# Optimization experiments

Hardware: AMD Instinct MI355X
Metric: run time of the kernel (lower is better)

## Reference

```python
import jax, jax.numpy as jnp
import numpy as np

D_MODEL, N_HEAD, D_FFN = 1024, 16, 4096
MAX_REL = 128
NUM_BUCKETS = 2 * MAX_REL - 1  # 255
B, T = 2, 2048


def algebraic_ln(x, gamma, beta, a, b_raw, eps=1e-5):
    mean = jnp.mean(x, axis=-1, keepdims=True)
    var = jnp.var(x, axis=-1, keepdims=True)  # unbiased=False
    z = var + eps
    b = jax.nn.softplus(10.0 * b_raw) / 10.0  # softplus with beta=10
    p = a[0] + a[1] * z + a[2] * z ** 2
    q = b[0] + b[1] * z + b[2] * z ** 2
    return (x - mean) * (p / q) * gamma + beta


def setup_inputs() -> dict:
    key = jax.random.key(0)
    ks = jax.random.split(key, 16)
    s = (1.0 / np.sqrt(D_MODEL)).astype(np.float32)
    inp = {
        'x': jax.random.normal(ks[0], (B, T, D_MODEL), jnp.float32),
        'casual_mask': jnp.tril(jnp.ones((T, T), dtype=bool)),
        'Wq': jax.random.normal(ks[1], (D_MODEL, D_MODEL), jnp.float32) * s,
        'bq': jnp.zeros((D_MODEL,), jnp.float32),
        'Wk': jax.random.normal(ks[2], (D_MODEL, D_MODEL), jnp.float32) * s,
        'bk': jnp.zeros((D_MODEL,), jnp.float32),
        'Wv': jax.random.normal(ks[3], (D_MODEL, D_MODEL), jnp.float32) * s,
        'bv': jnp.zeros((D_MODEL,), jnp.float32),
        'Wo': jax.random.normal(ks[4], (D_MODEL, D_MODEL), jnp.float32) * s,
        'bo': jnp.zeros((D_MODEL,), jnp.float32),
        'rel_emb': jax.random.normal(ks[5], (NUM_BUCKETS, N_HEAD), jnp.float32) * 0.02,
        'g1': jnp.ones((D_MODEL,), jnp.float32),
        'be1': jnp.zeros((D_MODEL,), jnp.float32),
        'a1': jnp.array([1.0, 0.5, 0.1], jnp.float32),
        'br1': jnp.array([1.0, 0.3, 0.05], jnp.float32),
        'g2': jnp.ones((D_MODEL,), jnp.float32),
        'be2': jnp.zeros((D_MODEL,), jnp.float32),
        'a2': jnp.array([1.0, 0.5, 0.1], jnp.float32),
        'br2': jnp.array([1.0, 0.3, 0.05], jnp.float32),
        'W1': jax.random.normal(ks[6], (D_FFN, D_MODEL), jnp.float32) * s,
        'b1': jnp.zeros((D_FFN,), jnp.float32),
        'W2': jax.random.normal(ks[7], (D_MODEL, D_FFN), jnp.float32) * (1.0 / np.sqrt(D_FFN)),
        'b2': jnp.zeros((D_MODEL,), jnp.float32),
        'res_scale': jnp.array(0.5, jnp.float32),
    }
    return inp


def attention(x, mask, Wq, bq, Wk, bk, Wv, bv, Wo, bo, rel_emb):
    Bx, Tx, C = x.shape
    H, Dh = N_HEAD, C // N_HEAD
    scale = Dh ** -0.5
    Q = (x @ Wq.T + bq).reshape(Bx, Tx, H, Dh)
    K = (x @ Wk.T + bk).reshape(Bx, Tx, H, Dh)
    V = (x @ Wv.T + bv).reshape(Bx, Tx, H, Dh)
    scores = jnp.einsum('bqhd,bkhd->bhqk', Q, K) * scale
    rel = jnp.arange(Tx)[None, :] - jnp.arange(Tx)[:, None]  # k_pos - q_pos
    buckets = jnp.clip(rel, -MAX_REL + 1, MAX_REL - 1) + (MAX_REL - 1)
    bias = rel_emb[buckets]  # [T,T,H]
    scores = scores + jnp.transpose(bias, (2, 0, 1))[None]
    m = mask[None, None]  # [1,1,T,T]
    # torch: masked_fill(-inf) then masked_fill(0) -> masked entries become 0
    scores = jnp.where(m, scores, 0.0)
    w = jax.nn.relu(scores) + 1e-6
    w = jnp.where(m, w, 0.0)
    w = w / (jnp.sum(w, axis=-1, keepdims=True) + 1e-6)
    out = jnp.einsum('bhqk,bkhd->bqhd', w, V).reshape(Bx, Tx, C)
    return out @ Wo.T + bo


def reference(x, casual_mask, Wq, bq, Wk, bk, Wv, bv, Wo, bo, rel_emb,
              g1, be1, a1, br1, g2, be2, a2, br2, W1, b1, W2, b2, res_scale):
    scale = jnp.clip(res_scale, 0.2, 1.0)
    x = x + scale * attention(algebraic_ln(x, g1, be1, a1, br1), casual_mask,
                              Wq, bq, Wk, bk, Wv, bv, Wo, bo, rel_emb)
    h = algebraic_ln(x, g2, be2, a2, br2)
    ffn = jax.nn.relu(h @ W1.T + b1) @ W2.T + b2  # dropout is identity at eval
    return x + scale * ffn
```

## Files before the change

kernel.cpp:

```cpp
#include <hip/hip_runtime.h>
#include <stdint.h>


#define D_MODEL 1024
#define T_SEQ   2048
#define NHEAD   16
#define DH      64
#define DFFN    4096
#define MROWS   4096

using short8  = __attribute__((ext_vector_type(8))) short;
using floatx4 = __attribute__((ext_vector_type(4))) float;

__device__ __forceinline__ float bf2f(ushort u) {
    union { uint32_t i; float f; } x; x.i = ((uint32_t)u) << 16; return x.f;
}
__device__ __forceinline__ ushort f2bf(float f) {
    union { float f; uint32_t i; } x; x.f = f;
    uint32_t i = x.i;
    return (ushort)((i + 0x7fffu + ((i >> 16) & 1u)) >> 16);
}
__device__ __forceinline__ float ldf(const void* p, size_t i, int dt) {
    return dt ? bf2f(((const ushort*)p)[i]) : ((const float*)p)[i];
}
__device__ __forceinline__ int detect_bf16(const void* g1) {
    return *(const uint32_t*)g1 == 0x3F803F80u;
}
__device__ __forceinline__ void gld_lds16(const void* g, void* l) {
    __builtin_amdgcn_global_load_lds(
        (__attribute__((address_space(1))) uint32_t*)(g),
        (__attribute__((address_space(3))) uint32_t*)(l), 16, 0, 0);
}
__device__ __forceinline__ float softplus10(float t) {
    float u = 10.f * t;
    return (u > 20.f ? u : log1pf(expf(u))) * 0.1f;
}

template <int INMODE>
__global__ __launch_bounds__(256)
void ln_kernel(const void* __restrict__ xin,
               const void* __restrict__ gamma, const void* __restrict__ beta,
               const void* __restrict__ a3, const void* __restrict__ br3,
               ushort* __restrict__ out, const void* __restrict__ dtprobe,
               const void* __restrict__ b2fold, const void* __restrict__ scale_p)
{
    const int dt = detect_bf16(dtprobe);
    const int row = blockIdx.x;
    const int tid = threadIdx.x;
    const int col = tid * 4;
    float v[4];
    if (INMODE >= 1) {
        const float* x = (const float*)xin + (size_t)row * D_MODEL;
        float4 t = *(const float4*)(x + col);
        v[0] = t.x; v[1] = t.y; v[2] = t.z; v[3] = t.w;
    } else if (dt) {
        const ushort* x = (const ushort*)xin + (size_t)row * D_MODEL;
        ushort4 t = *(const ushort4*)(x + col);
        v[0] = bf2f(t.x); v[1] = bf2f(t.y); v[2] = bf2f(t.z); v[3] = bf2f(t.w);
    } else {
        const float* x = (const float*)xin + (size_t)row * D_MODEL;
        float4 t = *(const float4*)(x + col);
        v[0] = t.x; v[1] = t.y; v[2] = t.z; v[3] = t.w;
    }
    float s  = v[0] + v[1] + v[2] + v[3];
    float s2 = v[0]*v[0] + v[1]*v[1] + v[2]*v[2] + v[3]*v[3];
#pragma unroll
    for (int m = 32; m > 0; m >>= 1) {
        s  += __shfl_down(s,  m, 64);
        s2 += __shfl_down(s2, m, 64);
    }
    __shared__ float wsum[4], wsum2[4];
    const int wave = tid >> 6, lane = tid & 63;
    if (lane == 0) { wsum[wave] = s; wsum2[wave] = s2; }
    __syncthreads();
    s  = wsum[0] + wsum[1] + wsum[2] + wsum[3];
    s2 = wsum2[0] + wsum2[1] + wsum2[2] + wsum2[3];
    const float mean = s * (1.f / D_MODEL);
    const float var  = s2 * (1.f / D_MODEL) - mean * mean;
    const float z = var + 1e-5f;
    const float a0 = ldf(a3, 0, dt), a1 = ldf(a3, 1, dt), a2 = ldf(a3, 2, dt);
    const float b0 = softplus10(ldf(br3, 0, dt));
    const float b1 = softplus10(ldf(br3, 1, dt));
    const float b2 = softplus10(ldf(br3, 2, dt));
    const float p = a0 + a1 * z + a2 * z * z;
    const float q = b0 + b1 * z + b2 * z * z;
    const float f = p / q;
    ushort4 o; ushort* op = (ushort*)&o;
#pragma unroll
    for (int e = 0; e < 4; e++) {
        op[e] = f2bf((v[e] - mean) * f * ldf(gamma, col + e, dt) + ldf(beta, col + e, dt));
    }
    *(ushort4*)(out + (size_t)row * D_MODEL + col) = o;
    if (INMODE == 2) {
        const float scl = fminf(fmaxf(ldf(scale_p, 0, dt), 0.2f), 1.0f);
        float* xw = (float*)xin + (size_t)row * D_MODEL;
        float4 t;
        t.x = v[0] + scl * ldf(b2fold, col + 0, dt);
        t.y = v[1] + scl * ldf(b2fold, col + 1, dt);
        t.z = v[2] + scl * ldf(b2fold, col + 2, dt);
        t.w = v[3] + scl * ldf(b2fold, col + 3, dt);
        *(float4*)(xw + col) = t;
    }
}

__global__ __launch_bounds__(256)
void cast_out(const float* __restrict__ x1, void* __restrict__ out,
              const void* __restrict__ dtprobe)
{
    const int dt = detect_bf16(dtprobe);
    const int row = blockIdx.x;
    const int col = threadIdx.x * 4;
    float4 t = *(const float4*)(x1 + (size_t)row * D_MODEL + col);
    if (dt) {
        ushort4 o;
        o.x = f2bf(t.x); o.y = f2bf(t.y); o.z = f2bf(t.z); o.w = f2bf(t.w);
        *(ushort4*)((ushort*)out + (size_t)row * D_MODEL + col) = o;
    } else {
        *(float4*)((float*)out + (size_t)row * D_MODEL + col) = t;
    }
}

template <int MODE, int BM, int BN>
__global__ __launch_bounds__(256)
void gemm_bt(const ushort* __restrict__ A,
             const void* __restrict__ Bw0, const void* __restrict__ Bw1,
             const void* __restrict__ Bw2,
             const void* __restrict__ bias0, const void* __restrict__ bias1,
             const void* __restrict__ bias2,
             void* __restrict__ C0, void* __restrict__ C1, void* __restrict__ C2v,
             int Nst, int K, const void* __restrict__ dtprobe)
{
    constexpr int NI = BM / 32;
    constexpr int NJ = BN / 32;
    constexpr int AC = BM / 64;
    constexpr int BC = BN / 64;
    __shared__ __align__(16) ushort As[BM * 32];
    __shared__ __align__(16) ushort Bs[BN * 32];
    const int dt = detect_bf16(dtprobe);
    const int tid  = threadIdx.x;
    const int wave = tid >> 6, lane = tid & 63;
    const int wr = wave >> 1, wc = wave & 1;
    const int g = lane >> 4, l15 = lane & 15;

    const void* Bw = Bw0; const void* bias = bias0; void* Cout = C0;
    if (MODE == 4) {
        const int mat = blockIdx.x >> 3;
        if (mat == 1)      { Bw = Bw1; bias = bias1; Cout = C1; }
        else if (mat == 2) { Bw = Bw2; bias = bias2; Cout = C2v; }
    }
    const int m0 = blockIdx.y * BM;
    const int n0 = (MODE == 4) ? ((blockIdx.x & 7) * 128) : (blockIdx.x * BN);

    floatx4 acc[NI][NJ];
#pragma unroll
    for (int i = 0; i < NI; i++)
#pragma unroll
        for (int j = 0; j < NJ; j++) acc[i][j] = {0.f, 0.f, 0.f, 0.f};

    const int srow = lane >> 2;
    const int ssw  = (srow >> 1) & 3;
    const int scol = (((lane & 3) ^ ssw) * 8);
    const int fsw  = (l15 >> 1) & 3;
    for (int k0 = 0; k0 < K; k0 += 32) {
        __syncthreads();
        if (dt) {
            const ushort* Bb = (const ushort*)Bw;
#pragma unroll
            for (int c = 0; c < AC; c++) {
                const int r0 = (wave * AC + c) * 16;
                gld_lds16(A + (size_t)(m0 + r0 + srow) * K + k0 + scol, &As[r0 * 32]);
            }
#pragma unroll
            for (int c = 0; c < BC; c++) {
                const int r0 = (wave * BC + c) * 16;
                gld_lds16(Bb + (size_t)(n0 + r0 + srow) * K + k0 + scol, &Bs[r0 * 32]);
            }
        } else {
            const float* Bf = (const float*)Bw;
#pragma unroll
            for (int c = 0; c < AC; c++) {
                const int r0 = (wave * AC + c) * 16;
                gld_lds16(A + (size_t)(m0 + r0 + srow) * K + k0 + scol, &As[r0 * 32]);
            }
#pragma unroll
            for (int c = 0; c < BC; c++) {
                const int r0 = (wave * BC + c) * 16;
                const float* src = Bf + (size_t)(n0 + r0 + srow) * K + k0 + scol;
                float4 t0 = *(const float4*)(src);
                float4 t1 = *(const float4*)(src + 4);
                ushort tmp[8] = { f2bf(t0.x), f2bf(t0.y), f2bf(t0.z), f2bf(t0.w),
                                  f2bf(t1.x), f2bf(t1.y), f2bf(t1.z), f2bf(t1.w) };
                *(short8*)&Bs[(r0 + srow) * 32 + (lane & 3) * 8] = *(short8*)tmp;
            }
        }
        __syncthreads();
        short8 af[NI], bfr[NJ];
#pragma unroll
        for (int i = 0; i < NI; i++)
            af[i]  = *(const short8*)&As[(wr * (BM / 2) + i * 16 + l15) * 32 + ((g ^ fsw) * 8)];
#pragma unroll
        for (int j = 0; j < NJ; j++)
            bfr[j] = *(const short8*)&Bs[(wc * (BN / 2) + j * 16 + l15) * 32 + ((g ^ fsw) * 8)];
#pragma unroll
        for (int i = 0; i < NI; i++)
#pragma unroll
            for (int j = 0; j < NJ; j++)
                acc[i][j] = __builtin_amdgcn_mfma_f32_16x16x32_bf16(af[i], bfr[j], acc[i][j], 0, 0, 0);
    }

#pragma unroll
    for (int i = 0; i < NI; i++) {
        const int rowb = m0 + wr * (BM / 2) + i * 16 + g * 4;
#pragma unroll
        for (int j = 0; j < NJ; j++) {
            const int col = n0 + wc * (BN / 2) + j * 16 + l15;
            const float bi = ldf(bias, col, dt);
#pragma unroll
            for (int r = 0; r < 4; r++) {
                const size_t idx = (size_t)(rowb + r) * Nst + col;
                const float v = acc[i][j][r] + bi;
                if (MODE == 1) ((ushort*)Cout)[idx] = f2bf(fmaxf(v, 0.f));
                else           ((ushort*)Cout)[idx] = f2bf(v);
            }
        }
    }
}

template <int MODE>
__global__ __launch_bounds__(256)
void gemm_k64p(const ushort* __restrict__ A, const void* __restrict__ Bw,
               const void* __restrict__ bias, void* __restrict__ Cout,
               const void* __restrict__ resid, const void* __restrict__ scale_p,
               int Nst, int K, const void* __restrict__ dtprobe)
{
    __shared__ __align__(16) ushort As[2][2][64 * 32];
    __shared__ __align__(16) ushort Bs[2][2][64 * 32];
    const int dt = detect_bf16(dtprobe);
    const int tid  = threadIdx.x;
    const int wave = tid >> 6, lane = tid & 63;
    const int wr = wave >> 1, wc = wave & 1;
    const int g = lane >> 4, l15 = lane & 15;
    const int m0 = blockIdx.y * 64, n0 = blockIdx.x * 64;

    floatx4 acc[2][2];
#pragma unroll
    for (int i = 0; i < 2; i++)
#pragma unroll
        for (int j = 0; j < 2; j++) acc[i][j] = {0.f, 0.f, 0.f, 0.f};

    const int srow = lane >> 2;
    const int ssw  = (srow >> 1) & 3;
    const int scol = (((lane & 3) ^ ssw) * 8);
    const int fsw  = (l15 >> 1) & 3;
    const int r0   = wave * 16;

    auto stage = [&](int buf, int k0) {
        if (dt) {
            const ushort* Bb = (const ushort*)Bw;
#pragma unroll
            for (int kb = 0; kb < 2; kb++) {
                gld_lds16(A  + (size_t)(m0 + r0 + srow) * K + k0 + kb * 32 + scol, &As[buf][kb][r0 * 32]);
                gld_lds16(Bb + (size_t)(n0 + r0 + srow) * K + k0 + kb * 32 + scol, &Bs[buf][kb][r0 * 32]);
            }
        } else {
            const float* Bf = (const float*)Bw;
#pragma unroll
            for (int kb = 0; kb < 2; kb++) {
                gld_lds16(A + (size_t)(m0 + r0 + srow) * K + k0 + kb * 32 + scol, &As[buf][kb][r0 * 32]);
                const float* src = Bf + (size_t)(n0 + r0 + srow) * K + k0 + kb * 32 + scol;
                float4 t0 = *(const float4*)(src);
                float4 t1 = *(const float4*)(src + 4);
                ushort tmp[8] = { f2bf(t0.x), f2bf(t0.y), f2bf(t0.z), f2bf(t0.w),
                                  f2bf(t1.x), f2bf(t1.y), f2bf(t1.z), f2bf(t1.w) };
                *(short8*)&Bs[buf][kb][(r0 + srow) * 32 + (lane & 3) * 8] = *(short8*)tmp;
            }
        }
    };

    const int nt = K >> 6;
    stage(0, 0);
    __syncthreads();
    int cur = 0;
    for (int t = 0; t < nt; ++t) {
        if (t + 1 < nt) stage(cur ^ 1, (t + 1) << 6);
        short8 af[2][2], bfr[2][2];
#pragma unroll
        for (int kb = 0; kb < 2; kb++) {
#pragma unroll
            for (int i = 0; i < 2; i++)
                af[i][kb]  = *(const short8*)&As[cur][kb][(wr * 32 + i * 16 + l15) * 32 + ((g ^ fsw) * 8)];
#pragma unroll
            for (int j = 0; j < 2; j++)
                bfr[j][kb] = *(const short8*)&Bs[cur][kb][(wc * 32 + j * 16 + l15) * 32 + ((g ^ fsw) * 8)];
        }
#pragma unroll
        for (int kb = 0; kb < 2; kb++)
#pragma unroll
            for (int i = 0; i < 2; i++)
#pragma unroll
                for (int j = 0; j < 2; j++)
                    acc[i][j] = __builtin_amdgcn_mfma_f32_16x16x32_bf16(af[i][kb], bfr[j][kb], acc[i][j], 0, 0, 0);
        __syncthreads();
        cur ^= 1;
    }

    const float scl = fminf(fmaxf(ldf(scale_p, 0, dt), 0.2f), 1.0f);
#pragma unroll
    for (int i = 0; i < 2; i++) {
        const int rowb = m0 + wr * 32 + i * 16 + g * 4;
#pragma unroll
        for (int j = 0; j < 2; j++) {
            const int col = n0 + wc * 32 + j * 16 + l15;
            const float bi = ldf(bias, col, dt);
#pragma unroll
            for (int r = 0; r < 4; r++) {
                const size_t idx = (size_t)(rowb + r) * Nst + col;
                const float v = acc[i][j][r] + bi;
                if (MODE == 2) ((float*)Cout)[idx] = ldf(resid, idx, dt) + scl * v;
                else {
                    const float o = ((const float*)resid)[idx] + scl * v;
                    if (dt) ((ushort*)Cout)[idx] = f2bf(o);
                    else    ((float*)Cout)[idx]  = o;
                }
            }
        }
    }
}

__global__ __launch_bounds__(256)
void gemm_k64s(const ushort* __restrict__ A, const void* __restrict__ Bw,
               float* __restrict__ Cacc, const void* __restrict__ scale_p,
               int Nst, int K, int kext, const void* __restrict__ dtprobe)
{
    __shared__ __align__(16) ushort As[2][64 * 32];
    __shared__ __align__(16) ushort Bs[2][64 * 32];
    const int dt = detect_bf16(dtprobe);
    const int tid  = threadIdx.x;
    const int wave = tid >> 6, lane = tid & 63;
    const int wr = wave >> 1, wc = wave & 1;
    const int g = lane >> 4, l15 = lane & 15;
    const int m0 = blockIdx.y * 64, n0 = blockIdx.x * 64;
    const int ks0 = blockIdx.z * kext;

    floatx4 acc[2][2];
#pragma unroll
    for (int i = 0; i < 2; i++)
#pragma unroll
        for (int j = 0; j < 2; j++) acc[i][j] = {0.f, 0.f, 0.f, 0.f};

    const int srow = lane >> 2;
    const int ssw  = (srow >> 1) & 3;
    const int scol = (((lane & 3) ^ ssw) * 8);
    const int fsw  = (l15 >> 1) & 3;
    const int r0   = wave * 16;

    for (int k0 = ks0; k0 < ks0 + kext; k0 += 64) {
        __syncthreads();
        if (dt) {
            const ushort* Bb = (const ushort*)Bw;
#pragma unroll
            for (int kb = 0; kb < 2; kb++) {
                gld_lds16(A  + (size_t)(m0 + r0 + srow) * K + k0 + kb * 32 + scol, &As[kb][r0 * 32]);
                gld_lds16(Bb + (size_t)(n0 + r0 + srow) * K + k0 + kb * 32 + scol, &Bs[kb][r0 * 32]);
            }
        } else {
            const float* Bf = (const float*)Bw;
#pragma unroll
            for (int kb = 0; kb < 2; kb++) {
                gld_lds16(A + (size_t)(m0 + r0 + srow) * K + k0 + kb * 32 + scol, &As[kb][r0 * 32]);
                const float* src = Bf + (size_t)(n0 + r0 + srow) * K + k0 + kb * 32 + scol;
                float4 t0 = *(const float4*)(src);
                float4 t1 = *(const float4*)(src + 4);
                ushort tmp[8] = { f2bf(t0.x), f2bf(t0.y), f2bf(t0.z), f2bf(t0.w),
                                  f2bf(t1.x), f2bf(t1.y), f2bf(t1.z), f2bf(t1.w) };
                *(short8*)&Bs[kb][(r0 + srow) * 32 + (lane & 3) * 8] = *(short8*)tmp;
            }
        }
        __syncthreads();
        short8 af[2][2], bfr[2][2];
#pragma unroll
        for (int kb = 0; kb < 2; kb++) {
#pragma unroll
            for (int i = 0; i < 2; i++)
                af[i][kb]  = *(const short8*)&As[kb][(wr * 32 + i * 16 + l15) * 32 + ((g ^ fsw) * 8)];
#pragma unroll
            for (int j = 0; j < 2; j++)
                bfr[j][kb] = *(const short8*)&Bs[kb][(wc * 32 + j * 16 + l15) * 32 + ((g ^ fsw) * 8)];
        }
#pragma unroll
        for (int kb = 0; kb < 2; kb++)
#pragma unroll
            for (int i = 0; i < 2; i++)
#pragma unroll
                for (int j = 0; j < 2; j++)
                    acc[i][j] = __builtin_amdgcn_mfma_f32_16x16x32_bf16(af[i][kb], bfr[j][kb], acc[i][j], 0, 0, 0);
    }

    const float scl = fminf(fmaxf(ldf(scale_p, 0, dt), 0.2f), 1.0f);
#pragma unroll
    for (int i = 0; i < 2; i++) {
        const int rowb = m0 + wr * 32 + i * 16 + g * 4;
#pragma unroll
        for (int j = 0; j < 2; j++) {
            const int col = n0 + wc * 32 + j * 16 + l15;
#pragma unroll
            for (int r = 0; r < 4; r++) {
                const size_t idx = (size_t)(rowb + r) * Nst + col;
                atomicAdd(&Cacc[idx], scl * acc[i][j][r]);
            }
        }
    }
}

__global__ __launch_bounds__(256)
void attn_kernel(const ushort* __restrict__ Q, const ushort* __restrict__ K,
                 const ushort* __restrict__ V, const void* __restrict__ rel,
                 ushort* __restrict__ Out, const void* __restrict__ dtprobe)
{
    __shared__ __align__(16) ushort Ks[64 * 64];
    __shared__ __align__(16) ushort Vt[64 * 88];
    __shared__ __align__(16) ushort Ss[64 * 88];
    __shared__ float rel_h[128];
    __shared__ float den_l[64];

    const int dt = detect_bf16(dtprobe);
    const int tid  = threadIdx.x;
    const int wave = tid >> 6, lane = tid & 63;
    const int wr = wave >> 1, wc = wave & 1;
    const int g = lane >> 4, l15 = lane & 15;
    const int pair = blockIdx.x, h = blockIdx.y, b = blockIdx.z;

    if (tid < 128) rel_h[tid] = ldf(rel, (size_t)tid * NHEAD + h, dt);
    const float scale = 0.125f;

    for (int ph = 0; ph < 2; ph++) {
        const int qt = ph ? (31 - pair) : pair;
        __syncthreads();
        if (tid < 64) den_l[tid] = 0.f;

        const ushort* Qg = Q + ((size_t)(b * T_SEQ + qt * 64)) * D_MODEL + h * DH;
        short8 qa[2][2];
#pragma unroll
        for (int i = 0; i < 2; i++)
#pragma unroll
            for (int ks = 0; ks < 2; ks++)
                qa[i][ks] = *(const short8*)(Qg + (size_t)(wr * 32 + i * 16 + l15) * D_MODEL
                                             + (ks * 4 + g) * 8);

        floatx4 onum[2][2];
#pragma unroll
        for (int i = 0; i < 2; i++) { onum[i][0] = {0.f,0.f,0.f,0.f}; onum[i][1] = {0.f,0.f,0.f,0.f}; }
        float den_p[2][4];
#pragma unroll
        for (int i = 0; i < 2; i++)
#pragma unroll
            for (int r = 0; r < 4; r++) den_p[i][r] = 0.f;

        const int nk = qt + 1;
        for (int kt = 0; kt < nk; kt++) {
            const int kbase = kt * 64;
            __syncthreads();
            const ushort* Kg = K + ((size_t)(b * T_SEQ + kbase)) * D_MODEL + h * DH;
            {
                const int lrow = lane >> 3, pch = lane & 7;
#pragma unroll
                for (int c = 0; c < 2; c++) {
                    const int r0 = (wave * 2 + c) * 8;
                    const int row = r0 + lrow;
                    gld_lds16(Kg + (size_t)row * D_MODEL + ((pch ^ (row & 7)) * 8), &Ks[r0 * 64]);
                }
            }
            const ushort* Vg = V + ((size_t)(b * T_SEQ + kbase)) * D_MODEL + h * DH;
#pragma unroll
            for (int c = 0; c < 2; c++) {
                const int chunk = tid + c * 256;
                const int krow = chunk >> 3;
                const int bb   = chunk & 7;
                short8 t = *(const short8*)(Vg + (size_t)krow * D_MODEL + bb * 8);
                ushort tmp[8]; *(short8*)tmp = t;
#pragma unroll
                for (int e = 0; e < 8; e++) {
                    const int ee = (e + bb) & 7;
                    Vt[(bb * 8 + ee) * 88 + krow] = tmp[ee];
                }
            }
            __syncthreads();

            floatx4 sacc[2][2];
#pragma unroll
            for (int i = 0; i < 2; i++) { sacc[i][0] = {0.f,0.f,0.f,0.f}; sacc[i][1] = {0.f,0.f,0.f,0.f}; }
#pragma unroll
            for (int ks = 0; ks < 2; ks++) {
                short8 kb[2];
                const int ch = ks * 4 + g;
#pragma unroll
                for (int j = 0; j < 2; j++) {
                    const int row = wc * 32 + j * 16 + l15;
                    kb[j] = *(const short8*)&Ks[row * 64 + ((ch ^ (row & 7)) * 8)];
                }
#pragma unroll
                for (int i = 0; i < 2; i++)
#pragma unroll
                    for (int j = 0; j < 2; j++)
                        sacc[i][j] = __builtin_amdgcn_mfma_f32_16x16x32_bf16(qa[i][ks], kb[j], sacc[i][j], 0, 0, 0);
            }

            const int dq = qt - kt;
            if (dq >= 3) {
                const float c0 = rel_h[0];
#pragma unroll
                for (int i = 0; i < 2; i++) {
                    const int qrow = wr * 32 + i * 16 + g * 4;
#pragma unroll
                    for (int j = 0; j < 2; j++) {
                        const int kcol = wc * 32 + j * 16 + l15;
#pragma unroll
                        for (int r = 0; r < 4; r++) {
                            const float w = fmaxf(sacc[i][j][r] * scale + c0, 0.f) + 1e-6f;
                            den_p[i][r] += w;
                            Ss[(qrow + r) * 88 + kcol] = f2bf(w);
                        }
                    }
                }
            } else {
#pragma unroll
                for (int i = 0; i < 2; i++) {
                    const int qrow = wr * 32 + i * 16 + g * 4;
#pragma unroll
                    for (int j = 0; j < 2; j++) {
                        const int kcol = wc * 32 + j * 16 + l15;
                        const int kg = kbase + kcol;
#pragma unroll
                        for (int r = 0; r < 4; r++) {
                            const int qg = qt * 64 + qrow + r;
                            const int d = qg - kg;
                            float w = 0.f;
                            if (d >= 0) {
                                const int bucket = 127 - (d < 127 ? d : 127);
                                const float sv = sacc[i][j][r] * scale + rel_h[bucket];
                                w = fmaxf(sv, 0.f) + 1e-6f;
                            }
                            den_p[i][r] += w;
                            Ss[(qrow + r) * 88 + kcol] = f2bf(w);
                        }
                    }
                }
            }
            __syncthreads();

#pragma unroll
            for (int ks = 0; ks < 2; ks++) {
                short8 wa[2], vb[2];
#pragma unroll
                for (int i = 0; i < 2; i++)
                    wa[i] = *(const short8*)&Ss[(wr * 32 + i * 16 + l15) * 88 + ks * 32 + g * 8];
#pragma unroll
                for (int j = 0; j < 2; j++)
                    vb[j] = *(const short8*)&Vt[(wc * 32 + j * 16 + l15) * 88 + ks * 32 + g * 8];
#pragma unroll
                for (int i = 0; i < 2; i++)
#pragma unroll
                    for (int j = 0; j < 2; j++)
                        onum[i][j] = __builtin_amdgcn_mfma_f32_16x16x32_bf16(wa[i], vb[j], onum[i][j], 0, 0, 0);
            }
        }

#pragma unroll
        for (int i = 0; i < 2; i++)
#pragma unroll
            for (int r = 0; r < 4; r++) {
                float v = den_p[i][r];
                v += __shfl_xor(v, 1, 64);
                v += __shfl_xor(v, 2, 64);
                v += __shfl_xor(v, 4, 64);
                v += __shfl_xor(v, 8, 64);
                den_p[i][r] = v;
            }
        __syncthreads();
        if (l15 == 0) {
#pragma unroll
            for (int i = 0; i < 2; i++)
#pragma unroll
                for (int r = 0; r < 4; r++)
                    atomicAdd(&den_l[wr * 32 + i * 16 + g * 4 + r], den_p[i][r]);
        }
        __syncthreads();

        const size_t obase = ((size_t)(b * T_SEQ + qt * 64)) * D_MODEL + h * DH;
#pragma unroll
        for (int i = 0; i < 2; i++) {
            const int qrow = wr * 32 + i * 16 + g * 4;
#pragma unroll
            for (int j = 0; j < 2; j++) {
                const int dcol = wc * 32 + j * 16 + l15;
#pragma unroll
                for (int r = 0; r < 4; r++) {
                    const float dn = den_l[qrow + r] + 1e-6f;
                    Out[obase + (size_t)(qrow + r) * D_MODEL + dcol] = f2bf(onum[i][j][r] / dn);
                }
            }
        }
    }
}

extern "C" void kernel_launch(void* const* d_in, const int* in_sizes, int n_in,
                              void* d_out, int out_size, void* d_ws, size_t ws_size,
                              hipStream_t stream)
{
    const void* x   = d_in[0];
    const void* Wq  = d_in[2];
    const void* bq  = d_in[3];
    const void* Wk  = d_in[4];
    const void* bk  = d_in[5];
    const void* Wv  = d_in[6];
    const void* bv  = d_in[7];
    const void* Wo  = d_in[8];
    const void* bo  = d_in[9];
    const void* rel = d_in[10];
    const void* g1  = d_in[11];
    const void* be1 = d_in[12];
    const void* a1  = d_in[13];
    const void* br1 = d_in[14];
    const void* g2  = d_in[15];
    const void* be2 = d_in[16];
    const void* a2  = d_in[17];
    const void* br2 = d_in[18];
    const void* W1  = d_in[19];
    const void* b1  = d_in[20];
    const void* W2  = d_in[21];
    const void* b2  = d_in[22];
    const void* rs  = d_in[23];

    char* ws = (char*)d_ws;
    ushort* ln1  = (ushort*)(ws);
    ushort* Qb   = (ushort*)(ws + (8u  << 20));
    ushort* Kb   = (ushort*)(ws + (16u << 20));
    ushort* Vb   = (ushort*)(ws + (24u << 20));
    ushort* atb  = (ushort*)(ws + (32u << 20));
    float*  x1   = (float*)(ws + (40u << 20));
    ushort* hbuf = (ushort*)(ws + (56u << 20));
    ushort* ffn1 = (ushort*)(ws);

    const dim3 blk(256);

    ln_kernel<0><<<dim3(MROWS), blk, 0, stream>>>(x, g1, be1, a1, br1, ln1, g1,
                                                  nullptr, nullptr);
    gemm_bt<4, 128, 128><<<dim3(24, MROWS / 128), blk, 0, stream>>>(
        ln1, Wq, Wk, Wv, bq, bk, bv, Qb, Kb, Vb, D_MODEL, D_MODEL, g1);
    attn_kernel<<<dim3(16, NHEAD, 2), blk, 0, stream>>>(Qb, Kb, Vb, rel, atb, g1);
    gemm_k64p<2><<<dim3(D_MODEL / 64, MROWS / 64), blk, 0, stream>>>(
        atb, Wo, bo, x1, x, rs, D_MODEL, D_MODEL, g1);
    ln_kernel<2><<<dim3(MROWS), blk, 0, stream>>>(x1, g2, be2, a2, br2, hbuf, g1,
                                                  b2, rs);
    gemm_bt<1, 128, 128><<<dim3(DFFN / 128, MROWS / 128), blk, 0, stream>>>(
        hbuf, W1, nullptr, nullptr, b1, nullptr, nullptr, ffn1, nullptr, nullptr,
        DFFN, D_MODEL, g1);
    gemm_k64s<<<dim3(D_MODEL / 64, MROWS / 64, 2), blk, 0, stream>>>(
        ffn1, W2, x1, rs, D_MODEL, DFFN, DFFN / 2, g1);
    cast_out<<<dim3(MROWS), blk, 0, stream>>>(x1, d_out, g1);
}
```

Measured before the change: 507.5 us.

## Split FFN down-projection K eight ways with flattened grid; drop Wo GEMM double buffering

The W2 GEMM goes from a 2-way to an 8-way split-K on a flattened 1D grid. Consecutive blocks now share an output tile across the K slices, which raises block count and should keep the same W2/A tiles close together in L2. It also relies on more atomic accumulation into x1, which means more atomic traffic. Separately, the Wo projection GEMM drops its double-buffered LDS prefetch for a single-buffer load-sync-compute loop, which uses less LDS but loses the overlap of loads with MFMA.

```diff
diff --git a/kernel.cpp b/kernel.cpp
--- a/kernel.cpp
+++ b/kernel.cpp
@@ -228,13 +228,13 @@
 
 template <int MODE>
 __global__ __launch_bounds__(256)
-void gemm_k64p(const ushort* __restrict__ A, const void* __restrict__ Bw,
-               const void* __restrict__ bias, void* __restrict__ Cout,
-               const void* __restrict__ resid, const void* __restrict__ scale_p,
-               int Nst, int K, const void* __restrict__ dtprobe)
+void gemm_k64(const ushort* __restrict__ A, const void* __restrict__ Bw,
+              const void* __restrict__ bias, void* __restrict__ Cout,
+              const void* __restrict__ resid, const void* __restrict__ scale_p,
+              int Nst, int K, const void* __restrict__ dtprobe)
 {
-    __shared__ __align__(16) ushort As[2][2][64 * 32];
-    __shared__ __align__(16) ushort Bs[2][2][64 * 32];
+    __shared__ __align__(16) ushort As[2][64 * 32];
+    __shared__ __align__(16) ushort Bs[2][64 * 32];
     const int dt = detect_bf16(dtprobe);
     const int tid  = threadIdx.x;
     const int wave = tid >> 6, lane = tid & 63;
@@ -254,44 +254,38 @@
     const int fsw  = (l15 >> 1) & 3;
     const int r0   = wave * 16;
 
-    auto stage = [&](int buf, int k0) {
+    for (int k0 = 0; k0 < K; k0 += 64) {
+        __syncthreads();
         if (dt) {
             const ushort* Bb = (const ushort*)Bw;
 #pragma unroll
             for (int kb = 0; kb < 2; kb++) {
-                gld_lds16(A  + (size_t)(m0 + r0 + srow) * K + k0 + kb * 32 + scol, &As[buf][kb][r0 * 32]);
-                gld_lds16(Bb + (size_t)(n0 + r0 + srow) * K + k0 + kb * 32 + scol, &Bs[buf][kb][r0 * 32]);
+                gld_lds16(A  + (size_t)(m0 + r0 + srow) * K + k0 + kb * 32 + scol, &As[kb][r0 * 32]);
+                gld_lds16(Bb + (size_t)(n0 + r0 + srow) * K + k0 + kb * 32 + scol, &Bs[kb][r0 * 32]);
             }
         } else {
             const float* Bf = (const float*)Bw;
 #pragma unroll
             for (int kb = 0; kb < 2; kb++) {
-                gld_lds16(A + (size_t)(m0 + r0 + srow) * K + k0 + kb * 32 + scol, &As[buf][kb][r0 * 32]);
+                gld_lds16(A + (size_t)(m0 + r0 + srow) * K + k0 + kb * 32 + scol, &As[kb][r0 * 32]);
                 const float* src = Bf + (size_t)(n0 + r0 + srow) * K + k0 + kb * 32 + scol;
                 float4 t0 = *(const float4*)(src);
                 float4 t1 = *(const float4*)(src + 4);
                 ushort tmp[8] = { f2bf(t0.x), f2bf(t0.y), f2bf(t0.z), f2bf(t0.w),
                                   f2bf(t1.x), f2bf(t1.y), f2bf(t1.z), f2bf(t1.w) };
-                *(short8*)&Bs[buf][kb][(r0 + srow) * 32 + (lane & 3) * 8] = *(short8*)tmp;
-            }
-        }
-    };
-
-    const int nt = K >> 6;
-    stage(0, 0);
-    __syncthreads();
-    int cur = 0;
-    for (int t = 0; t < nt; ++t) {
-        if (t + 1 < nt) stage(cur ^ 1, (t + 1) << 6);
+                *(short8*)&Bs[kb][(r0 + srow) * 32 + (lane & 3) * 8] = *(short8*)tmp;
+            }
+        }
+        __syncthreads();
         short8 af[2][2], bfr[2][2];
 #pragma unroll
         for (int kb = 0; kb < 2; kb++) {
 #pragma unroll
             for (int i = 0; i < 2; i++)
-                af[i][kb]  = *(const short8*)&As[cur][kb][(wr * 32 + i * 16 + l15) * 32 + ((g ^ fsw) * 8)];
+                af[i][kb]  = *(const short8*)&As[kb][(wr * 32 + i * 16 + l15) * 32 + ((g ^ fsw) * 8)];
 #pragma unroll
             for (int j = 0; j < 2; j++)
-                bfr[j][kb] = *(const short8*)&Bs[cur][kb][(wc * 32 + j * 16 + l15) * 32 + ((g ^ fsw) * 8)];
+                bfr[j][kb] = *(const short8*)&Bs[kb][(wc * 32 + j * 16 + l15) * 32 + ((g ^ fsw) * 8)];
         }
 #pragma unroll
         for (int kb = 0; kb < 2; kb++)
@@ -300,8 +294,6 @@
 #pragma unroll
                 for (int j = 0; j < 2; j++)
                     acc[i][j] = __builtin_amdgcn_mfma_f32_16x16x32_bf16(af[i][kb], bfr[j][kb], acc[i][j], 0, 0, 0);
-        __syncthreads();
-        cur ^= 1;
     }
 
     const float scl = fminf(fmaxf(ldf(scale_p, 0, dt), 0.2f), 1.0f);
@@ -328,9 +320,9 @@
 }
 
 __global__ __launch_bounds__(256)
-void gemm_k64s(const ushort* __restrict__ A, const void* __restrict__ Bw,
-               float* __restrict__ Cacc, const void* __restrict__ scale_p,
-               int Nst, int K, int kext, const void* __restrict__ dtprobe)
+void gemm_skx(const ushort* __restrict__ A, const void* __restrict__ Bw,
+              float* __restrict__ Cacc, const void* __restrict__ scale_p,
+              int Nst, int K, int kext, const void* __restrict__ dtprobe)
 {
     __shared__ __align__(16) ushort As[2][64 * 32];
     __shared__ __align__(16) ushort Bs[2][64 * 32];
@@ -339,8 +331,13 @@
     const int wave = tid >> 6, lane = tid & 63;
     const int wr = wave >> 1, wc = wave & 1;
     const int g = lane >> 4, l15 = lane & 15;
-    const int m0 = blockIdx.y * 64, n0 = blockIdx.x * 64;
-    const int ks0 = blockIdx.z * kext;
+
+    const int fid = blockIdx.x;
+    const int zsl = fid & 7;
+    const int nb  = (fid >> 3) & 15;
+    const int mb  = fid >> 7;
+    const int m0 = mb * 64, n0 = nb * 64;
+    const int ks0 = zsl * kext;
 
     floatx4 acc[2][2];
 #pragma unroll
@@ -648,14 +645,14 @@
     gemm_bt<4, 128, 128><<<dim3(24, MROWS / 128), blk, 0, stream>>>(
         ln1, Wq, Wk, Wv, bq, bk, bv, Qb, Kb, Vb, D_MODEL, D_MODEL, g1);
     attn_kernel<<<dim3(16, NHEAD, 2), blk, 0, stream>>>(Qb, Kb, Vb, rel, atb, g1);
-    gemm_k64p<2><<<dim3(D_MODEL / 64, MROWS / 64), blk, 0, stream>>>(
+    gemm_k64<2><<<dim3(D_MODEL / 64, MROWS / 64), blk, 0, stream>>>(
         atb, Wo, bo, x1, x, rs, D_MODEL, D_MODEL, g1);
     ln_kernel<2><<<dim3(MROWS), blk, 0, stream>>>(x1, g2, be2, a2, br2, hbuf, g1,
                                                   b2, rs);
     gemm_bt<1, 128, 128><<<dim3(DFFN / 128, MROWS / 128), blk, 0, stream>>>(
         hbuf, W1, nullptr, nullptr, b1, nullptr, nullptr, ffn1, nullptr, nullptr,
         DFFN, D_MODEL, g1);
-    gemm_k64s<<<dim3(D_MODEL / 64, MROWS / 64, 2), blk, 0, stream>>>(
-        ffn1, W2, x1, rs, D_MODEL, DFFN, DFFN / 2, g1);
+    gemm_skx<<<dim3(64 * 16 * 8), blk, 0, stream>>>(
+        ffn1, W2, x1, rs, D_MODEL, DFFN, DFFN / 8, g1);
     cast_out<<<dim3(MROWS), blk, 0, stream>>>(x1, d_out, g1);
 }
```

Result: slower. 528.1 us (+4.1%).
